# Kernel tuning notes

Hardware: AMD Instinct MI355X
Metric: run time of the kernel (lower is better)

## Reference

```python
import jax, jax.numpy as jnp
import numpy as np

V = 20000      # nodes
L = 4          # topological levels
PER = 5000     # nodes per level
DEG = 16       # parents per node
D = 512        # d_model
H = 8          # nheads
Cd = D // H    # head_dim
E = (L - 1) * PER * DEG


def setup_inputs() -> dict:
    rng = np.random.default_rng(0)
    node_levels = np.repeat(np.arange(L), PER).astype(np.int64)
    srcs, tgts = [], []
    for l in range(1, L):
        srcs.append(rng.integers((l - 1) * PER, l * PER, size=PER * DEG))
        tgts.append(np.repeat(np.arange(l * PER, (l + 1) * PER), DEG))
    edge_index = np.stack([np.concatenate(srcs), np.concatenate(tgts)]).astype(np.int64)
    key = jax.random.key(0)
    ks = jax.random.split(key, 14)
    glorot = 0.05
    def p(k, shape):
        return jax.random.normal(k, shape, jnp.float32) * glorot
    return {
        'node_feats': jax.random.normal(ks[0], (V, D), jnp.float32),
        'edge_feats': jax.random.normal(ks[1], (E, D), jnp.float32),
        'edge_index': jnp.asarray(edge_index),
        'node_levels': jnp.asarray(node_levels),
        'n_levels': L,
        'Wn_bu': p(ks[2], (D, D)), 'We_bu': p(ks[3], (D, D)), 'attn_bu': p(ks[4], (H, 3 * Cd)),
        'Wo_bu': p(ks[5], (D, D)), 'bo_bu': jnp.zeros((D,), jnp.float32),
        'Wn_td': p(ks[6], (D, D)), 'We_td': p(ks[7], (D, D)), 'attn_td': p(ks[8], (H, 3 * Cd)),
        'Wo_td': p(ks[9], (D, D)), 'bo_td': jnp.zeros((D,), jnp.float32),
    }


def _direction(node_feats, edge_feats, Wn, We, attn_w, Wo, bo, src, tgt, node_lv, n_levels):
    Vn = node_feats.shape[0]
    scale = (3 * Cd) ** -0.5
    aw_j, aw_i, aw_e = attn_w[:, :Cd], attn_w[:, Cd:2 * Cd], attn_w[:, 2 * Cd:]
    # edge features are static across levels -> project once
    ep = (edge_feats @ We).reshape(-1, H, Cd)            # E h c
    ep_alpha = jnp.einsum('ehc,hc->eh', ep, aw_e)        # E h
    edge_lv = node_lv[tgt]                               # level of each edge's target
    for l in range(1, n_levels):
        xp = (node_feats @ Wn).reshape(Vn, H, Cd)        # V h c
        aj = jnp.einsum('vhc,hc->vh', xp, aw_j)
        ai = jnp.einsum('vhc,hc->vh', xp, aw_i)
        a = (aj[src] + ai[tgt] + ep_alpha) * scale       # E h
        a = jnp.where((edge_lv == l)[:, None], a, -jnp.inf)
        # self-loop: edge feature filled with 0.0 -> only x_j/x_i terms
        sa = (aj + ai) * scale                           # V h
        m = jnp.maximum(jax.ops.segment_max(a, tgt, num_segments=Vn), sa)
        we = jnp.exp(a - m[tgt])                         # E h (0 for masked edges)
        ws = jnp.exp(sa - m)                             # V h
        denom = jax.ops.segment_sum(we, tgt, num_segments=Vn) + ws
        agg = jax.ops.segment_sum(we[:, :, None] * xp[src], tgt, num_segments=Vn) + ws[:, :, None] * xp
        out = (agg / denom[:, :, None]).reshape(Vn, H * Cd) @ Wo + bo  # to_out (dropout=eval identity)
        node_feats = jnp.where((node_lv == l)[:, None], out, node_feats)
    return node_feats


def reference(node_feats, edge_feats, edge_index, node_levels, n_levels,
              Wn_bu, We_bu, attn_bu, Wo_bu, bo_bu,
              Wn_td, We_td, attn_td, Wo_td, bo_td):
    src, tgt = edge_index[0], edge_index[1]
    # bottom-up: edges as given, topo levels 0..L-1
    bu = _direction(node_feats, edge_feats, Wn_bu, We_bu, attn_bu, Wo_bu, bo_bu,
                    src, tgt, node_levels, n_levels)
    # top-down: reversed edges, topo levels reversed
    lv_td = (n_levels - 1) - node_levels
    td = _direction(node_feats, edge_feats, Wn_td, We_td, attn_td, Wo_td, bo_td,
                    tgt, src, lv_td, n_levels)
    return jnp.stack([td, bu], axis=0)  # (topdown, bottomup)
```

## Files before the change

### kernel.cpp

```cpp
#include <hip/hip_runtime.h>

#define NV 20000
#define NE 240000
#define PER 5000
#define DEG 16
#define EPB 80000
#define SCALE 0.07216878364870323f
#define MAXDEG 96

typedef __attribute__((ext_vector_type(8))) short s16x8;
typedef __attribute__((ext_vector_type(4))) float f32x4;

__device__ inline ushort bf16rne(float x) {
    uint32_t u = __float_as_uint(x);
    u += 0x7fffu + ((u >> 16) & 1u);
    return (ushort)(u >> 16);
}
__device__ inline s16x8 cvt8(float4 a, float4 b) {
    s16x8 v;
    v[0] = (short)bf16rne(a.x); v[1] = (short)bf16rne(a.y);
    v[2] = (short)bf16rne(a.z); v[3] = (short)bf16rne(a.w);
    v[4] = (short)bf16rne(b.x); v[5] = (short)bf16rne(b.y);
    v[6] = (short)bf16rne(b.z); v[7] = (short)bf16rne(b.w);
    return v;
}

__global__ void init_copy(const float* __restrict__ nf, float* __restrict__ out) {
    int i = blockIdx.x * 256 + threadIdx.x;
    float4 v = reinterpret_cast<const float4*>(nf)[i];
    reinterpret_cast<float4*>(out)[i] = v;
    reinterpret_cast<float4*>(out + (size_t)NV * 512)[i] = v;
}

__global__ void fold_kernel(
    const float* __restrict__ Wn_bu, const float* __restrict__ attn_bu,
    const float* __restrict__ Wn_td, const float* __restrict__ attn_td,
    const float* __restrict__ We_bu, const float* __restrict__ We_td,
    ushort* __restrict__ Bt1_bu, ushort* __restrict__ Bt1_td,
    ushort* __restrict__ foldE)
{
    int idx = blockIdx.x * 256 + threadIdx.x;
    const int SZ = 64 * 512;
    if (idx < 2 * SZ) {
        int arr = idx / SZ;
        int r = idx - arr * SZ;
        int o = r >> 9;
        int d = r & 511;
        ushort val = 0;
        if (o < 16) {
            const float* W    = arr ? Wn_td   : Wn_bu;
            const float* attn = arr ? attn_td : attn_bu;
            int h = o & 7;
            int awOff = (o < 8) ? 0 : 64;
            float s = 0.f;
            for (int cc = 0; cc < 64; ++cc)
                s += W[d * 512 + h * 64 + cc] * attn[h * 192 + awOff + cc];
            val = bf16rne(s);
        }
        (arr ? Bt1_td : Bt1_bu)[(size_t)(512 + o) * 512 + d] = val;
    } else if (idx < 2 * SZ + 16 * 512) {
        int r = idx - 2 * SZ;
        int o = r >> 9;
        int d = r & 511;
        const float* W    = (o < 8) ? We_bu   : We_td;
        const float* attn = (o < 8) ? attn_bu : attn_td;
        int h = o & 7;
        float s = 0.f;
        for (int cc = 0; cc < 64; ++cc)
            s += W[d * 512 + h * 64 + cc] * attn[h * 192 + 128 + cc];
        foldE[o * 512 + d] = bf16rne(s);
    }
}

__global__ __launch_bounds__(256) void prep_w(
    const float* __restrict__ W0, const float* __restrict__ W1,
    const float* __restrict__ W2, const float* __restrict__ W3,
    ushort* __restrict__ Bt1_bu, ushort* __restrict__ Bt2_bu,
    ushort* __restrict__ Bt1_td, ushort* __restrict__ Bt2_td)
{
    __shared__ float T[64][65];
    const int t = threadIdx.x;
    const int b = blockIdx.x;
    const int mat = b >> 6;
    const int tk = (b >> 3) & 7, tn = b & 7;
    const float* W = (mat == 0) ? W0 : (mat == 1) ? W1 : (mat == 2) ? W2 : W3;
    ushort* outp = (mat == 0) ? Bt1_bu : (mat == 1) ? Bt2_bu : (mat == 2) ? Bt1_td : Bt2_td;
    const int k0 = tk * 64, n0 = tn * 64;
    #pragma unroll
    for (int i = 0; i < 4; ++i) {
        int r = (t >> 4) * 4 + i;
        int c = (t & 15) * 4;
        float4 v = *reinterpret_cast<const float4*>(W + (size_t)(k0 + r) * 512 + n0 + c);
        T[r][c + 0] = v.x; T[r][c + 1] = v.y; T[r][c + 2] = v.z; T[r][c + 3] = v.w;
    }
    __syncthreads();
    #pragma unroll
    for (int i = 0; i < 4; ++i) {
        int n = (t >> 4) * 4 + i;
        int c = (t & 15) * 4;
        ushort4 o;
        o.x = bf16rne(T[c + 0][n]); o.y = bf16rne(T[c + 1][n]);
        o.z = bf16rne(T[c + 2][n]); o.w = bf16rne(T[c + 3][n]);
        *reinterpret_cast<ushort4*>(outp + (size_t)(n0 + n) * 512 + k0 + c) = o;
    }
}

__global__ __launch_bounds__(256) void rowdot_mfma(
    const float* __restrict__ A, int nTiles,
    const ushort* __restrict__ Bt16, float* __restrict__ out)
{
    __shared__ ushort Bs[16][520];
    const int t = threadIdx.x;
    for (int i = t; i < 16 * 512; i += 256)
        Bs[i >> 9][i & 511] = Bt16[i];
    __syncthreads();
    const int wave = t >> 6, lane = t & 63;
    const int tile = blockIdx.x * 4 + wave;
    if (tile >= nTiles) return;
    const int fr = lane & 15;
    const int fk = (lane >> 4) * 8;
    const float* Ar = A + (size_t)tile * 16 * 512 + (size_t)fr * 512;
    f32x4 acc = {0.f, 0.f, 0.f, 0.f};
    #pragma unroll
    for (int k0 = 0; k0 < 512; k0 += 32) {
        float4 a0 = *reinterpret_cast<const float4*>(Ar + k0 + fk);
        float4 a1 = *reinterpret_cast<const float4*>(Ar + k0 + fk + 4);
        s16x8 av = cvt8(a0, a1);
        s16x8 bv = *reinterpret_cast<const s16x8*>(&Bs[fr][k0 + fk]);
        acc = __builtin_amdgcn_mfma_f32_16x16x32_bf16(av, bv, acc, 0, 0, 0);
    }
    #pragma unroll
    for (int i = 0; i < 4; ++i) {
        int r = tile * 16 + (lane >> 4) * 4 + i;
        out[(size_t)r * 16 + (lane & 15)] = acc[i];
    }
}

__global__ __launch_bounds__(256) void gemm1_fused(
    const float* __restrict__ Abu, const float* __restrict__ Atd,
    const ushort* __restrict__ Btbu, const ushort* __restrict__ Bttd,
    float* __restrict__ xpbu, float* __restrict__ xptd,
    float* __restrict__ ajbu, float* __restrict__ ajtd)
{
    __shared__ ushort As[64][40];
    __shared__ ushort Bs[64][40];
    const int z = blockIdx.z;
    const float* A   = z ? Atd  : Abu;
    const ushort* Bt = z ? Bttd : Btbu;
    float* xp = z ? xptd : xpbu;
    float* aj = z ? ajtd : ajbu;
    const int M = 10000;
    const int t = threadIdx.x;
    const int wave = t >> 6, lane = t & 63;
    const int row0 = blockIdx.x * 64, col0 = blockIdx.y * 64;
    const int wm = (wave >> 1) * 32, wn = (wave & 1) * 32;
    const int sm = t >> 2;
    const int sk = (t & 3) * 8;
    const int fr = lane & 15;
    const int fk = (lane >> 4) * 8;
    const bool aok = (row0 + sm) < M;
    const float* Ap = A + (size_t)(row0 + sm) * 512;
    const ushort* Bp = Bt + (size_t)(col0 + sm) * 512;
    f32x4 acc[2][2];
    #pragma unroll
    for (int mi = 0; mi < 2; ++mi)
        #pragma unroll
        for (int ni = 0; ni < 2; ++ni) acc[mi][ni] = (f32x4){0.f, 0.f, 0.f, 0.f};

    for (int k0 = 0; k0 < 512; k0 += 32) {
        float4 a0, a1;
        if (aok) {
            a0 = *reinterpret_cast<const float4*>(Ap + k0 + sk);
            a1 = *reinterpret_cast<const float4*>(Ap + k0 + sk + 4);
        } else {
            a0 = make_float4(0.f, 0.f, 0.f, 0.f);
            a1 = a0;
        }
        *reinterpret_cast<s16x8*>(&As[sm][sk]) = cvt8(a0, a1);
        *reinterpret_cast<s16x8*>(&Bs[sm][sk]) =
            *reinterpret_cast<const s16x8*>(Bp + k0 + sk);
        __syncthreads();
        s16x8 af[2], bf[2];
        af[0] = *reinterpret_cast<const s16x8*>(&As[wm + fr][fk]);
        af[1] = *reinterpret_cast<const s16x8*>(&As[wm + 16 + fr][fk]);
        bf[0] = *reinterpret_cast<const s16x8*>(&Bs[wn + fr][fk]);
        bf[1] = *reinterpret_cast<const s16x8*>(&Bs[wn + 16 + fr][fk]);
        acc[0][0] = __builtin_amdgcn_mfma_f32_16x16x32_bf16(af[0], bf[0], acc[0][0], 0, 0, 0);
        acc[0][1] = __builtin_amdgcn_mfma_f32_16x16x32_bf16(af[0], bf[1], acc[0][1], 0, 0, 0);
        acc[1][0] = __builtin_amdgcn_mfma_f32_16x16x32_bf16(af[1], bf[0], acc[1][0], 0, 0, 0);
        acc[1][1] = __builtin_amdgcn_mfma_f32_16x16x32_bf16(af[1], bf[1], acc[1][1], 0, 0, 0);
        __syncthreads();
    }
    #pragma unroll
    for (int mi = 0; mi < 2; ++mi) {
        #pragma unroll
        for (int ni = 0; ni < 2; ++ni) {
            int c = col0 + wn + ni * 16 + (lane & 15);
            #pragma unroll
            for (int i = 0; i < 4; ++i) {
                int r = row0 + wm + mi * 16 + (lane >> 4) * 4 + i;
                if (r < M) {
                    if (c < 512)       xp[(size_t)r * 512 + c] = acc[mi][ni][i];
                    else if (c < 528)  aj[(size_t)r * 16 + (c - 512)] = acc[mi][ni][i];
                }
            }
        }
    }
}

__global__ __launch_bounds__(256) void gemm2_fused(
    const float* __restrict__ Abu, const float* __restrict__ Atd,
    const ushort* __restrict__ Btbu, const ushort* __restrict__ Bttd,
    float* __restrict__ Cbu, float* __restrict__ Ctd,
    const float* __restrict__ bbu, const float* __restrict__ btd)
{
    __shared__ ushort As[64][40];
    __shared__ ushort Bs[64][40];
    const int z = blockIdx.z;
    const float* A   = z ? Atd  : Abu;
    const ushort* Bt = z ? Bttd : Btbu;
    float* C = z ? Ctd : Cbu;
    const float* bias = z ? btd : bbu;
    const int M = 5000;
    const int t = threadIdx.x;
    const int wave = t >> 6, lane = t & 63;
    const int row0 = blockIdx.x * 64, col0 = blockIdx.y * 64;
    const int wm = (wave >> 1) * 32, wn = (wave & 1) * 32;
    const int sm = t >> 2;
    const int sk = (t & 3) * 8;
    const int fr = lane & 15;
    const int fk = (lane >> 4) * 8;
    const bool aok = (row0 + sm) < M;
    const float* Ap = A + (size_t)(row0 + sm) * 512;
    const ushort* Bp = Bt + (size_t)(col0 + sm) * 512;
    f32x4 acc[2][2];
    #pragma unroll
    for (int mi = 0; mi < 2; ++mi)
        #pragma unroll
        for (int ni = 0; ni < 2; ++ni) acc[mi][ni] = (f32x4){0.f, 0.f, 0.f, 0.f};

    for (int k0 = 0; k0 < 512; k0 += 32) {
        float4 a0, a1;
        if (aok) {
            a0 = *reinterpret_cast<const float4*>(Ap + k0 + sk);
            a1 = *reinterpret_cast<const float4*>(Ap + k0 + sk + 4);
        } else {
            a0 = make_float4(0.f, 0.f, 0.f, 0.f);
            a1 = a0;
        }
        *reinterpret_cast<s16x8*>(&As[sm][sk]) = cvt8(a0, a1);
        *reinterpret_cast<s16x8*>(&Bs[sm][sk]) =
            *reinterpret_cast<const s16x8*>(Bp + k0 + sk);
        __syncthreads();
        s16x8 af[2], bf[2];
        af[0] = *reinterpret_cast<const s16x8*>(&As[wm + fr][fk]);
        af[1] = *reinterpret_cast<const s16x8*>(&As[wm + 16 + fr][fk]);
        bf[0] = *reinterpret_cast<const s16x8*>(&Bs[wn + fr][fk]);
        bf[1] = *reinterpret_cast<const s16x8*>(&Bs[wn + 16 + fr][fk]);
        acc[0][0] = __builtin_amdgcn_mfma_f32_16x16x32_bf16(af[0], bf[0], acc[0][0], 0, 0, 0);
        acc[0][1] = __builtin_amdgcn_mfma_f32_16x16x32_bf16(af[0], bf[1], acc[0][1], 0, 0, 0);
        acc[1][0] = __builtin_amdgcn_mfma_f32_16x16x32_bf16(af[1], bf[0], acc[1][0], 0, 0, 0);
        acc[1][1] = __builtin_amdgcn_mfma_f32_16x16x32_bf16(af[1], bf[1], acc[1][1], 0, 0, 0);
        __syncthreads();
    }
    #pragma unroll
    for (int mi = 0; mi < 2; ++mi) {
        #pragma unroll
        for (int ni = 0; ni < 2; ++ni) {
            int c = col0 + wn + ni * 16 + (lane & 15);
            float bb = bias[c];
            #pragma unroll
            for (int i = 0; i < 4; ++i) {
                int r = row0 + wm + mi * 16 + (lane >> 4) * 4 + i;
                if (r < M) C[(size_t)r * 512 + c] = acc[mi][ni][i] + bb;
            }
        }
    }
}

__global__ void csr_zero(int* cnt) {
    int i = blockIdx.x * 256 + threadIdx.x;
    if (i < 15000) cnt[i] = 0;
}
__global__ void csr_count(const int* __restrict__ ei, int* __restrict__ cnt) {
    int e = blockIdx.x * 256 + threadIdx.x;
    if (e >= NE) return;
    int lv = e / EPB;
    int local = ei[e] - lv * PER;
    atomicAdd(&cnt[lv * PER + local], 1);
}
__global__ void csr_scan(const int* __restrict__ cnt, int* __restrict__ rptr,
                         int* __restrict__ off) {
    __shared__ int part[256];
    int lv = blockIdx.x, t = threadIdx.x;
    int s = 0;
    if (t < 250)
        for (int j = 0; j < 20; ++j) s += cnt[lv * PER + t * 20 + j];
    part[t] = s;
    __syncthreads();
    if (t == 0) {
        int run = 0;
        for (int i = 0; i < 250; ++i) { int v = part[i]; part[i] = run; run += v; }
        rptr[lv * 5001 + 5000] = run;
    }
    __syncthreads();
    if (t < 250) {
        int run = part[t];
        for (int j = 0; j < 20; ++j) {
            int idx = t * 20 + j;
            rptr[lv * 5001 + idx] = run;
            off[lv * PER + idx] = run;
            run += cnt[lv * PER + idx];
        }
    }
}
__global__ void csr_fill(const int* __restrict__ ei, int* __restrict__ off, int* __restrict__ eids) {
    int e = blockIdx.x * 256 + threadIdx.x;
    if (e >= NE) return;
    int lv = e / EPB;
    int local = ei[e] - lv * PER;
    int pos = atomicAdd(&off[lv * PER + local], 1);
    eids[lv * EPB + pos] = e;
}

__global__ __launch_bounds__(512) void attn_fused(
    const float* __restrict__ xp_bu, const float* __restrict__ ajai_bu,
    const float* __restrict__ xp_td, const float* __restrict__ ajai_td,
    const float* __restrict__ epA,
    const int* __restrict__ ei_src, const int* __restrict__ ei_tgt,
    const int* __restrict__ rptr,
    const int* __restrict__ eids,
    int eBaseBU, int baseBU, int baseTD,
    float* __restrict__ aggn_bu, float* __restrict__ aggn_td)
{
    __shared__ float Lwe[4][MAXDEG][8];
    __shared__ int   Lsrci[4][MAXDEG];
    __shared__ float Lws[4][8];
    __shared__ float Ldenom[4][8];
    const int tid = threadIdx.x;
    const int q = tid >> 7, f = tid & 127;
    const bool isBU = blockIdx.x < 1250;
    const int t = (isBU ? blockIdx.x : blockIdx.x - 1250) * 4 + q;

    const float* xp   = isBU ? xp_bu   : xp_td;
    const float* ajai = isBU ? ajai_bu : ajai_td;
    const int* srcArr = isBU ? ei_src  : ei_tgt;
    const int base    = isBU ? baseBU  : baseTD;
    const int tgtXp   = (isBU ? 5000 : 0) + t;
    const int dirOff  = isBU ? 0 : 8;
    float* aggn       = isBU ? aggn_bu : aggn_td;

    int deg, ebase;
    if (isBU) { deg = DEG; ebase = eBaseBU + t * DEG; }
    else      { int r0 = rptr[t]; deg = rptr[t + 1] - r0; ebase = r0; }
    if (deg > MAXDEG) deg = MAXDEG;

    const float tAi = ajai[tgtXp * 16 + 8 + (f & 7)];
    for (int kk = f; kk < deg * 8; kk += 128) {
        int k = kk >> 3, h = kk & 7;
        int e = isBU ? (ebase + k) : eids[ebase + k];
        int src = srcArr[e] - base;
        float lg = (ajai[src * 16 + h] + tAi + epA[(size_t)e * 16 + dirOff + h]) * SCALE;
        Lwe[q][k][h] = lg;
        if (h == 0) Lsrci[q][k] = src;
    }
    if (f < 8) Lws[q][f] = (ajai[tgtXp * 16 + f] + ajai[tgtXp * 16 + 8 + f]) * SCALE;
    __syncthreads();
    if (f < 8) {
        float m = Lws[q][f];
        for (int k = 0; k < deg; ++k) m = fmaxf(m, Lwe[q][k][f]);
        float dsum = 0.f;
        for (int k = 0; k < deg; ++k) {
            float w = expf(Lwe[q][k][f] - m);
            Lwe[q][k][f] = w;
            dsum += w;
        }
        float wsv = expf(Lws[q][f] - m);
        Lws[q][f] = wsv;
        Ldenom[q][f] = dsum + wsv;
    }
    __syncthreads();
    const int h = f >> 4;
    const float4* xp4 = reinterpret_cast<const float4*>(xp);
    float4 xv = xp4[(size_t)tgtXp * 128 + f];
    float w0 = Lws[q][h];
    float ax = w0 * xv.x, ay = w0 * xv.y, az = w0 * xv.z, aw = w0 * xv.w;
    if (isBU) {
        #pragma unroll
        for (int k = 0; k < DEG; ++k) {
            float w = Lwe[q][k][h];
            float4 v = xp4[(size_t)Lsrci[q][k] * 128 + f];
            ax += w * v.x; ay += w * v.y; az += w * v.z; aw += w * v.w;
        }
    } else {
        #pragma unroll 4
        for (int k = 0; k < deg; ++k) {
            float w = Lwe[q][k][h];
            float4 v = xp4[(size_t)Lsrci[q][k] * 128 + f];
            ax += w * v.x; ay += w * v.y; az += w * v.z; aw += w * v.w;
        }
    }
    float inv = 1.f / Ldenom[q][h];
    float4 r; r.x = ax * inv; r.y = ay * inv; r.z = az * inv; r.w = aw * inv;
    reinterpret_cast<float4*>(aggn)[(size_t)t * 128 + f] = r;
}

extern "C" void kernel_launch(void* const* d_in, const int* in_sizes, int n_in,
                              void* d_out, int out_size, void* d_ws, size_t ws_size,
                              hipStream_t stream) {
    const float* node_feats = (const float*)d_in[0];
    const float* edge_feats = (const float*)d_in[1];
    const int*   edge_index = (const int*)d_in[2];
    const float* Wn_bu  = (const float*)d_in[5];
    const float* We_bu  = (const float*)d_in[6];
    const float* attn_bu = (const float*)d_in[7];
    const float* Wo_bu  = (const float*)d_in[8];
    const float* bo_bu  = (const float*)d_in[9];
    const float* Wn_td  = (const float*)d_in[10];
    const float* We_td  = (const float*)d_in[11];
    const float* attn_td = (const float*)d_in[12];
    const float* Wo_td  = (const float*)d_in[13];
    const float* bo_td  = (const float*)d_in[14];

    float* out = (float*)d_out;
    float* td = out;
    float* bu = out + (size_t)NV * 512;

    float* ws      = (float*)d_ws;
    float* xp_bu   = ws;
    float* xp_td   = xp_bu + 5120000;
    float* aggn_bu = xp_td + 5120000;
    float* aggn_td = aggn_bu + 2560000;
    float* ajai_bu = aggn_td + 2560000;
    float* ajai_td = ajai_bu + 160000;
    float* epA     = ajai_td + 160000;
    int* cnt  = (int*)(epA + 3840000);
    int* off  = cnt + 15000;
    int* rptr = off + 15000;
    int* eids = rptr + 15008;
    ushort* Bt1_bu = (ushort*)(eids + 240000);
    ushort* Bt1_td = Bt1_bu + 294912;
    ushort* Bt2_bu = Bt1_td + 294912;
    ushort* Bt2_td = Bt2_bu + 262144;
    ushort* foldE  = Bt2_td + 262144;

    const int* ei_src = edge_index;
    const int* ei_tgt = edge_index + NE;

    init_copy<<<10000, 256, 0, stream>>>(node_feats, out);
    fold_kernel<<<288, 256, 0, stream>>>(Wn_bu, attn_bu, Wn_td, attn_td, We_bu, We_td,
                                         Bt1_bu, Bt1_td, foldE);
    prep_w<<<256, 256, 0, stream>>>(Wn_bu, Wo_bu, Wn_td, Wo_td,
                                    Bt1_bu, Bt2_bu, Bt1_td, Bt2_td);
    rowdot_mfma<<<3750, 256, 0, stream>>>(edge_feats, 15000, foldE, epA);

    csr_zero<<<59, 256, 0, stream>>>(cnt);
    csr_count<<<938, 256, 0, stream>>>(ei_src, cnt);
    csr_scan<<<3, 256, 0, stream>>>(cnt, rptr, off);
    csr_fill<<<938, 256, 0, stream>>>(ei_src, off, eids);

    for (int i = 1; i <= 3; ++i) {
        const int l = i, lvIdx = 3 - i;
        const int baseBU = (l - 1) * PER;
        const int baseTD = lvIdx * PER;
        gemm1_fused<<<dim3(157, 9, 2), 256, 0, stream>>>(
            bu + (size_t)baseBU * 512, td + (size_t)baseTD * 512,
            Bt1_bu, Bt1_td, xp_bu, xp_td, ajai_bu, ajai_td);
        attn_fused<<<2500, 512, 0, stream>>>(
            xp_bu, ajai_bu, xp_td, ajai_td, epA, ei_src, ei_tgt,
            rptr + lvIdx * 5001, eids + (size_t)lvIdx * EPB,
            (l - 1) * EPB, baseBU, baseTD, aggn_bu, aggn_td);
        gemm2_fused<<<dim3(79, 8, 2), 256, 0, stream>>>(
            aggn_bu, aggn_td, Bt2_bu, Bt2_td,
            bu + (size_t)l * PER * 512, td + (size_t)baseTD * 512,
            bo_bu, bo_td);
    }
}
```

Before: 1.172 ms.

## Use 128x128 bf16-input GEMM tiles with bf16 node mirrors and parallel softmax

Replaces the 64x64 fp32-input GEMMs with a templated 128x128 tile kernel that reads pre-converted bf16 operands into XOR-swizzled shared memory with a 64-wide K step. Node features are mirrored in bf16 (written in init_copy and in the output GEMM epilogue), and attention aggregates are stored as bf16, so the GEMMs no longer convert on load and move half the bytes. The per-target softmax now runs across 16 lanes per head using shuffles instead of 8 serial threads. The cost is extra bf16 mirror buffers and stores, plus a larger register footprint per thread that may reduce occupancy.

```diff
diff --git a/kernel.cpp b/kernel.cpp
--- a/kernel.cpp
+++ b/kernel.cpp
@@ -16,20 +16,17 @@
     u += 0x7fffu + ((u >> 16) & 1u);
     return (ushort)(u >> 16);
 }
-__device__ inline s16x8 cvt8(float4 a, float4 b) {
-    s16x8 v;
-    v[0] = (short)bf16rne(a.x); v[1] = (short)bf16rne(a.y);
-    v[2] = (short)bf16rne(a.z); v[3] = (short)bf16rne(a.w);
-    v[4] = (short)bf16rne(b.x); v[5] = (short)bf16rne(b.y);
-    v[6] = (short)bf16rne(b.z); v[7] = (short)bf16rne(b.w);
-    return v;
-}
-
-__global__ void init_copy(const float* __restrict__ nf, float* __restrict__ out) {
+
+__global__ void init_copy(const float* __restrict__ nf, float* __restrict__ out,
+                          ushort* __restrict__ mbu, ushort* __restrict__ mtd) {
     int i = blockIdx.x * 256 + threadIdx.x;
     float4 v = reinterpret_cast<const float4*>(nf)[i];
     reinterpret_cast<float4*>(out)[i] = v;
     reinterpret_cast<float4*>(out + (size_t)NV * 512)[i] = v;
+    ushort4 m;
+    m.x = bf16rne(v.x); m.y = bf16rne(v.y); m.z = bf16rne(v.z); m.w = bf16rne(v.w);
+    reinterpret_cast<ushort4*>(mbu)[i] = m;
+    reinterpret_cast<ushort4*>(mtd)[i] = m;
 }
 
 __global__ void fold_kernel(
@@ -40,7 +37,7 @@
     ushort* __restrict__ foldE)
 {
     int idx = blockIdx.x * 256 + threadIdx.x;
-    const int SZ = 64 * 512;
+    const int SZ = 128 * 512;
     if (idx < 2 * SZ) {
         int arr = idx / SZ;
         int r = idx - arr * SZ;
@@ -125,7 +122,11 @@
     for (int k0 = 0; k0 < 512; k0 += 32) {
         float4 a0 = *reinterpret_cast<const float4*>(Ar + k0 + fk);
         float4 a1 = *reinterpret_cast<const float4*>(Ar + k0 + fk + 4);
-        s16x8 av = cvt8(a0, a1);
+        s16x8 av;
+        av[0] = (short)bf16rne(a0.x); av[1] = (short)bf16rne(a0.y);
+        av[2] = (short)bf16rne(a0.z); av[3] = (short)bf16rne(a0.w);
+        av[4] = (short)bf16rne(a1.x); av[5] = (short)bf16rne(a1.y);
+        av[6] = (short)bf16rne(a1.z); av[7] = (short)bf16rne(a1.w);
         s16x8 bv = *reinterpret_cast<const s16x8*>(&Bs[fr][k0 + fk]);
         acc = __builtin_amdgcn_mfma_f32_16x16x32_bf16(av, bv, acc, 0, 0, 0);
     }
@@ -136,143 +137,115 @@
     }
 }
 
-__global__ __launch_bounds__(256) void gemm1_fused(
-    const float* __restrict__ Abu, const float* __restrict__ Atd,
+template<int MODE>
+__global__ __launch_bounds__(256) void gemm128(
+    const ushort* __restrict__ Abu, const ushort* __restrict__ Atd,
     const ushort* __restrict__ Btbu, const ushort* __restrict__ Bttd,
-    float* __restrict__ xpbu, float* __restrict__ xptd,
-    float* __restrict__ ajbu, float* __restrict__ ajtd)
+    int M,
+    float* __restrict__ f0bu, float* __restrict__ f0td,
+    float* __restrict__ f1bu, float* __restrict__ f1td,
+    ushort* __restrict__ mbu, ushort* __restrict__ mtd,
+    const float* __restrict__ bbu, const float* __restrict__ btd)
 {
-    __shared__ ushort As[64][40];
-    __shared__ ushort Bs[64][40];
+    __shared__ ushort As[128 * 64];
+    __shared__ ushort Bs[128 * 64];
     const int z = blockIdx.z;
-    const float* A   = z ? Atd  : Abu;
+    const ushort* A  = z ? Atd  : Abu;
     const ushort* Bt = z ? Bttd : Btbu;
-    float* xp = z ? xptd : xpbu;
-    float* aj = z ? ajtd : ajbu;
-    const int M = 10000;
     const int t = threadIdx.x;
     const int wave = t >> 6, lane = t & 63;
-    const int row0 = blockIdx.x * 64, col0 = blockIdx.y * 64;
-    const int wm = (wave >> 1) * 32, wn = (wave & 1) * 32;
-    const int sm = t >> 2;
-    const int sk = (t & 3) * 8;
+    const int row0 = blockIdx.x * 128, col0 = blockIdx.y * 128;
+    const int wm = (wave >> 1) * 64, wn = (wave & 1) * 64;
     const int fr = lane & 15;
-    const int fk = (lane >> 4) * 8;
-    const bool aok = (row0 + sm) < M;
-    const float* Ap = A + (size_t)(row0 + sm) * 512;
-    const ushort* Bp = Bt + (size_t)(col0 + sm) * 512;
-    f32x4 acc[2][2];
-    #pragma unroll
-    for (int mi = 0; mi < 2; ++mi)
-        #pragma unroll
-        for (int ni = 0; ni < 2; ++ni) acc[mi][ni] = (f32x4){0.f, 0.f, 0.f, 0.f};
-
-    for (int k0 = 0; k0 < 512; k0 += 32) {
-        float4 a0, a1;
-        if (aok) {
-            a0 = *reinterpret_cast<const float4*>(Ap + k0 + sk);
-            a1 = *reinterpret_cast<const float4*>(Ap + k0 + sk + 4);
-        } else {
-            a0 = make_float4(0.f, 0.f, 0.f, 0.f);
-            a1 = a0;
-        }
-        *reinterpret_cast<s16x8*>(&As[sm][sk]) = cvt8(a0, a1);
-        *reinterpret_cast<s16x8*>(&Bs[sm][sk]) =
-            *reinterpret_cast<const s16x8*>(Bp + k0 + sk);
+    const int fkg = lane >> 4;
+
+    f32x4 acc[4][4];
+    #pragma unroll
+    for (int mi = 0; mi < 4; ++mi)
+        #pragma unroll
+        for (int ni = 0; ni < 4; ++ni) acc[mi][ni] = (f32x4){0.f, 0.f, 0.f, 0.f};
+
+    for (int k0 = 0; k0 < 512; k0 += 64) {
+        s16x8 ra[4], rb[4];
+        #pragma unroll
+        for (int j = 0; j < 4; ++j) {
+            int g = t + 256 * j;
+            int r = g >> 3, sl = g & 7;
+            ra[j] = *reinterpret_cast<const s16x8*>(A  + (size_t)(row0 + r) * 512 + k0 + sl * 8);
+            rb[j] = *reinterpret_cast<const s16x8*>(Bt + (size_t)(col0 + r) * 512 + k0 + sl * 8);
+        }
         __syncthreads();
-        s16x8 af[2], bf[2];
-        af[0] = *reinterpret_cast<const s16x8*>(&As[wm + fr][fk]);
-        af[1] = *reinterpret_cast<const s16x8*>(&As[wm + 16 + fr][fk]);
-        bf[0] = *reinterpret_cast<const s16x8*>(&Bs[wn + fr][fk]);
-        bf[1] = *reinterpret_cast<const s16x8*>(&Bs[wn + 16 + fr][fk]);
-        acc[0][0] = __builtin_amdgcn_mfma_f32_16x16x32_bf16(af[0], bf[0], acc[0][0], 0, 0, 0);
-        acc[0][1] = __builtin_amdgcn_mfma_f32_16x16x32_bf16(af[0], bf[1], acc[0][1], 0, 0, 0);
-        acc[1][0] = __builtin_amdgcn_mfma_f32_16x16x32_bf16(af[1], bf[0], acc[1][0], 0, 0, 0);
-        acc[1][1] = __builtin_amdgcn_mfma_f32_16x16x32_bf16(af[1], bf[1], acc[1][1], 0, 0, 0);
+        #pragma unroll
+        for (int j = 0; j < 4; ++j) {
+            int g = t + 256 * j;
+            int r = g >> 3, sl = g & 7;
+            int so = (sl ^ (r & 7)) * 8;
+            *reinterpret_cast<s16x8*>(&As[r * 64 + so]) = ra[j];
+            *reinterpret_cast<s16x8*>(&Bs[r * 64 + so]) = rb[j];
+        }
         __syncthreads();
-    }
-    #pragma unroll
-    for (int mi = 0; mi < 2; ++mi) {
-        #pragma unroll
-        for (int ni = 0; ni < 2; ++ni) {
-            int c = col0 + wn + ni * 16 + (lane & 15);
+        #pragma unroll
+        for (int ks = 0; ks < 2; ++ks) {
+            s16x8 av[4], bv[4];
             #pragma unroll
-            for (int i = 0; i < 4; ++i) {
-                int r = row0 + wm + mi * 16 + (lane >> 4) * 4 + i;
-                if (r < M) {
-                    if (c < 512)       xp[(size_t)r * 512 + c] = acc[mi][ni][i];
-                    else if (c < 528)  aj[(size_t)r * 16 + (c - 512)] = acc[mi][ni][i];
+            for (int mi = 0; mi < 4; ++mi) {
+                int row = wm + mi * 16 + fr;
+                int cg = ks * 4 + fkg;
+                av[mi] = *reinterpret_cast<const s16x8*>(&As[row * 64 + ((cg ^ (row & 7)) * 8)]);
+            }
+            #pragma unroll
+            for (int ni = 0; ni < 4; ++ni) {
+                int row = wn + ni * 16 + fr;
+                int cg = ks * 4 + fkg;
+                bv[ni] = *reinterpret_cast<const s16x8*>(&Bs[row * 64 + ((cg ^ (row & 7)) * 8)]);
+            }
+            #pragma unroll
+            for (int mi = 0; mi < 4; ++mi)
+                #pragma unroll
+                for (int ni = 0; ni < 4; ++ni)
+                    acc[mi][ni] = __builtin_amdgcn_mfma_f32_16x16x32_bf16(av[mi], bv[ni], acc[mi][ni], 0, 0, 0);
+        }
+        __syncthreads();
+    }
+
+    if (MODE == 0) {
+        float* xp = z ? f0td : f0bu;
+        float* aj = z ? f1td : f1bu;
+        #pragma unroll
+        for (int mi = 0; mi < 4; ++mi) {
+            #pragma unroll
+            for (int ni = 0; ni < 4; ++ni) {
+                int c = col0 + wn + ni * 16 + (lane & 15);
+                #pragma unroll
+                for (int i = 0; i < 4; ++i) {
+                    int r = row0 + wm + mi * 16 + (lane >> 4) * 4 + i;
+                    if (r < M) {
+                        float v = acc[mi][ni][i];
+                        if (c < 512)      xp[(size_t)r * 512 + c] = v;
+                        else if (c < 528) aj[(size_t)r * 16 + (c - 512)] = v;
+                    }
                 }
             }
         }
-    }
-}
-
-__global__ __launch_bounds__(256) void gemm2_fused(
-    const float* __restrict__ Abu, const float* __restrict__ Atd,
-    const ushort* __restrict__ Btbu, const ushort* __restrict__ Bttd,
-    float* __restrict__ Cbu, float* __restrict__ Ctd,
-    const float* __restrict__ bbu, const float* __restrict__ btd)
-{
-    __shared__ ushort As[64][40];
-    __shared__ ushort Bs[64][40];
-    const int z = blockIdx.z;
-    const float* A   = z ? Atd  : Abu;
-    const ushort* Bt = z ? Bttd : Btbu;
-    float* C = z ? Ctd : Cbu;
-    const float* bias = z ? btd : bbu;
-    const int M = 5000;
-    const int t = threadIdx.x;
-    const int wave = t >> 6, lane = t & 63;
-    const int row0 = blockIdx.x * 64, col0 = blockIdx.y * 64;
-    const int wm = (wave >> 1) * 32, wn = (wave & 1) * 32;
-    const int sm = t >> 2;
-    const int sk = (t & 3) * 8;
-    const int fr = lane & 15;
-    const int fk = (lane >> 4) * 8;
-    const bool aok = (row0 + sm) < M;
-    const float* Ap = A + (size_t)(row0 + sm) * 512;
-    const ushort* Bp = Bt + (size_t)(col0 + sm) * 512;
-    f32x4 acc[2][2];
-    #pragma unroll
-    for (int mi = 0; mi < 2; ++mi)
-        #pragma unroll
-        for (int ni = 0; ni < 2; ++ni) acc[mi][ni] = (f32x4){0.f, 0.f, 0.f, 0.f};
-
-    for (int k0 = 0; k0 < 512; k0 += 32) {
-        float4 a0, a1;
-        if (aok) {
-            a0 = *reinterpret_cast<const float4*>(Ap + k0 + sk);
-            a1 = *reinterpret_cast<const float4*>(Ap + k0 + sk + 4);
-        } else {
-            a0 = make_float4(0.f, 0.f, 0.f, 0.f);
-            a1 = a0;
-        }
-        *reinterpret_cast<s16x8*>(&As[sm][sk]) = cvt8(a0, a1);
-        *reinterpret_cast<s16x8*>(&Bs[sm][sk]) =
-            *reinterpret_cast<const s16x8*>(Bp + k0 + sk);
-        __syncthreads();
-        s16x8 af[2], bf[2];
-        af[0] = *reinterpret_cast<const s16x8*>(&As[wm + fr][fk]);
-        af[1] = *reinterpret_cast<const s16x8*>(&As[wm + 16 + fr][fk]);
-        bf[0] = *reinterpret_cast<const s16x8*>(&Bs[wn + fr][fk]);
-        bf[1] = *reinterpret_cast<const s16x8*>(&Bs[wn + 16 + fr][fk]);
-        acc[0][0] = __builtin_amdgcn_mfma_f32_16x16x32_bf16(af[0], bf[0], acc[0][0], 0, 0, 0);
-        acc[0][1] = __builtin_amdgcn_mfma_f32_16x16x32_bf16(af[0], bf[1], acc[0][1], 0, 0, 0);
-        acc[1][0] = __builtin_amdgcn_mfma_f32_16x16x32_bf16(af[1], bf[0], acc[1][0], 0, 0, 0);
-        acc[1][1] = __builtin_amdgcn_mfma_f32_16x16x32_bf16(af[1], bf[1], acc[1][1], 0, 0, 0);
-        __syncthreads();
-    }
-    #pragma unroll
-    for (int mi = 0; mi < 2; ++mi) {
-        #pragma unroll
-        for (int ni = 0; ni < 2; ++ni) {
-            int c = col0 + wn + ni * 16 + (lane & 15);
-            float bb = bias[c];
+    } else {
+        float* C = z ? f0td : f0bu;
+        ushort* mir = z ? mtd : mbu;
+        const float* bias = z ? btd : bbu;
+        #pragma unroll
+        for (int mi = 0; mi < 4; ++mi) {
             #pragma unroll
-            for (int i = 0; i < 4; ++i) {
-                int r = row0 + wm + mi * 16 + (lane >> 4) * 4 + i;
-                if (r < M) C[(size_t)r * 512 + c] = acc[mi][ni][i] + bb;
+            for (int ni = 0; ni < 4; ++ni) {
+                int c = col0 + wn + ni * 16 + (lane & 15);
+                float bb = bias[c];
+                #pragma unroll
+                for (int i = 0; i < 4; ++i) {
+                    int r = row0 + wm + mi * 16 + (lane >> 4) * 4 + i;
+                    if (r < M) {
+                        float v = acc[mi][ni][i] + bb;
+                        C[(size_t)r * 512 + c] = v;
+                        mir[(size_t)r * 512 + c] = bf16rne(v);
+                    }
+                }
             }
         }
     }
@@ -331,12 +304,10 @@
     const int* __restrict__ rptr,
     const int* __restrict__ eids,
     int eBaseBU, int baseBU, int baseTD,
-    float* __restrict__ aggn_bu, float* __restrict__ aggn_td)
+    ushort* __restrict__ aggn_bu, ushort* __restrict__ aggn_td)
 {
     __shared__ float Lwe[4][MAXDEG][8];
     __shared__ int   Lsrci[4][MAXDEG];
-    __shared__ float Lws[4][8];
-    __shared__ float Ldenom[4][8];
     const int tid = threadIdx.x;
     const int q = tid >> 7, f = tid & 127;
     const bool isBU = blockIdx.x < 1250;
@@ -348,7 +319,7 @@
     const int base    = isBU ? baseBU  : baseTD;
     const int tgtXp   = (isBU ? 5000 : 0) + t;
     const int dirOff  = isBU ? 0 : 8;
-    float* aggn       = isBU ? aggn_bu : aggn_td;
+    ushort* aggn      = isBU ? aggn_bu : aggn_td;
 
     int deg, ebase;
     if (isBU) { deg = DEG; ebase = eBaseBU + t * DEG; }
@@ -364,27 +335,29 @@
         Lwe[q][k][h] = lg;
         if (h == 0) Lsrci[q][k] = src;
     }
-    if (f < 8) Lws[q][f] = (ajai[tgtXp * 16 + f] + ajai[tgtXp * 16 + 8 + f]) * SCALE;
-    __syncthreads();
-    if (f < 8) {
-        float m = Lws[q][f];
-        for (int k = 0; k < deg; ++k) m = fmaxf(m, Lwe[q][k][f]);
-        float dsum = 0.f;
-        for (int k = 0; k < deg; ++k) {
-            float w = expf(Lwe[q][k][f] - m);
-            Lwe[q][k][f] = w;
-            dsum += w;
-        }
-        float wsv = expf(Lws[q][f] - m);
-        Lws[q][f] = wsv;
-        Ldenom[q][f] = dsum + wsv;
-    }
-    __syncthreads();
-    const int h = f >> 4;
+    __syncthreads();
+
+    const int h = f >> 4, s = f & 15;
+    float sa = (ajai[tgtXp * 16 + h] + ajai[tgtXp * 16 + 8 + h]) * SCALE;
+    float m = sa;
+    for (int k = s; k < deg; k += 16) m = fmaxf(m, Lwe[q][k][h]);
+    #pragma unroll
+    for (int mk = 1; mk < 16; mk <<= 1) m = fmaxf(m, __shfl_xor(m, mk, 16));
+    float dsum = 0.f;
+    for (int k = s; k < deg; k += 16) {
+        float w = expf(Lwe[q][k][h] - m);
+        Lwe[q][k][h] = w;
+        dsum += w;
+    }
+    #pragma unroll
+    for (int mk = 1; mk < 16; mk <<= 1) dsum += __shfl_xor(dsum, mk, 16);
+    const float wsv = expf(sa - m);
+    const float inv = 1.f / (dsum + wsv);
+    __syncthreads();
+
     const float4* xp4 = reinterpret_cast<const float4*>(xp);
     float4 xv = xp4[(size_t)tgtXp * 128 + f];
-    float w0 = Lws[q][h];
-    float ax = w0 * xv.x, ay = w0 * xv.y, az = w0 * xv.z, aw = w0 * xv.w;
+    float ax = wsv * xv.x, ay = wsv * xv.y, az = wsv * xv.z, aw = wsv * xv.w;
     if (isBU) {
         #pragma unroll
         for (int k = 0; k < DEG; ++k) {
@@ -400,9 +373,10 @@
             ax += w * v.x; ay += w * v.y; az += w * v.z; aw += w * v.w;
         }
     }
-    float inv = 1.f / Ldenom[q][h];
-    float4 r; r.x = ax * inv; r.y = ay * inv; r.z = az * inv; r.w = aw * inv;
-    reinterpret_cast<float4*>(aggn)[(size_t)t * 128 + f] = r;
+    ushort4 o;
+    o.x = bf16rne(ax * inv); o.y = bf16rne(ay * inv);
+    o.z = bf16rne(az * inv); o.w = bf16rne(aw * inv);
+    *reinterpret_cast<ushort4*>(aggn + (size_t)t * 512 + f * 4) = o;
 }
 
 extern "C" void kernel_launch(void* const* d_in, const int* in_sizes, int n_in,
@@ -429,26 +403,28 @@
     float* ws      = (float*)d_ws;
     float* xp_bu   = ws;
     float* xp_td   = xp_bu + 5120000;
-    float* aggn_bu = xp_td + 5120000;
-    float* aggn_td = aggn_bu + 2560000;
-    float* ajai_bu = aggn_td + 2560000;
+    float* ajai_bu = xp_td + 5120000;
     float* ajai_td = ajai_bu + 160000;
     float* epA     = ajai_td + 160000;
     int* cnt  = (int*)(epA + 3840000);
     int* off  = cnt + 15000;
     int* rptr = off + 15000;
     int* eids = rptr + 15008;
-    ushort* Bt1_bu = (ushort*)(eids + 240000);
-    ushort* Bt1_td = Bt1_bu + 294912;
-    ushort* Bt2_bu = Bt1_td + 294912;
-    ushort* Bt2_td = Bt2_bu + 262144;
-    ushort* foldE  = Bt2_td + 262144;
+    ushort* aggn_bu = (ushort*)(eids + 240000);
+    ushort* aggn_td = aggn_bu + 2621440;
+    ushort* nf_bu   = aggn_td + 2621440;
+    ushort* nf_td   = nf_bu + 10321920;
+    ushort* Bt1_bu  = nf_td + 10321920;
+    ushort* Bt1_td  = Bt1_bu + 327680;
+    ushort* Bt2_bu  = Bt1_td + 327680;
+    ushort* Bt2_td  = Bt2_bu + 262144;
+    ushort* foldE   = Bt2_td + 262144;
 
     const int* ei_src = edge_index;
     const int* ei_tgt = edge_index + NE;
 
-    init_copy<<<10000, 256, 0, stream>>>(node_feats, out);
-    fold_kernel<<<288, 256, 0, stream>>>(Wn_bu, attn_bu, Wn_td, attn_td, We_bu, We_td,
+    init_copy<<<10000, 256, 0, stream>>>(node_feats, out, nf_bu, nf_td);
+    fold_kernel<<<544, 256, 0, stream>>>(Wn_bu, attn_bu, Wn_td, attn_td, We_bu, We_td,
                                          Bt1_bu, Bt1_td, foldE);
     prep_w<<<256, 256, 0, stream>>>(Wn_bu, Wo_bu, Wn_td, Wo_td,
                                     Bt1_bu, Bt2_bu, Bt1_td, Bt2_td);
@@ -463,16 +439,20 @@
         const int l = i, lvIdx = 3 - i;
         const int baseBU = (l - 1) * PER;
         const int baseTD = lvIdx * PER;
-        gemm1_fused<<<dim3(157, 9, 2), 256, 0, stream>>>(
-            bu + (size_t)baseBU * 512, td + (size_t)baseTD * 512,
-            Bt1_bu, Bt1_td, xp_bu, xp_td, ajai_bu, ajai_td);
+        gemm128<0><<<dim3(79, 5, 2), 256, 0, stream>>>(
+            nf_bu + (size_t)baseBU * 512, nf_td + (size_t)baseTD * 512,
+            Bt1_bu, Bt1_td, 10000,
+            xp_bu, xp_td, ajai_bu, ajai_td,
+            nullptr, nullptr, nullptr, nullptr);
         attn_fused<<<2500, 512, 0, stream>>>(
             xp_bu, ajai_bu, xp_td, ajai_td, epA, ei_src, ei_tgt,
             rptr + lvIdx * 5001, eids + (size_t)lvIdx * EPB,
             (l - 1) * EPB, baseBU, baseTD, aggn_bu, aggn_td);
-        gemm2_fused<<<dim3(79, 8, 2), 256, 0, stream>>>(
-            aggn_bu, aggn_td, Bt2_bu, Bt2_td,
+        gemm128<1><<<dim3(40, 4, 2), 256, 0, stream>>>(
+            aggn_bu, aggn_td, Bt2_bu, Bt2_td, 5000,
             bu + (size_t)l * PER * 512, td + (size_t)baseTD * 512,
+            nullptr, nullptr,
+            nf_bu + (size_t)l * PER * 512, nf_td + (size_t)baseTD * 512,
             bo_bu, bo_td);
     }
 }
```

After: 1.081 ms. 7.8% less time.
